# Optimization experiments

Measured on AMD Instinct MI355X. Metric: run time of the kernel, lower is better.

## Reference

```python
import jax, jax.numpy as jnp
import numpy as np

# Fixed feature layout standing in for config.group_tensor_index
IDX_LINE, IDX_LX, IDX_LY, IDX_RX, IDX_RY = 0, 1, 2, 3, 4

B, D, ROUND_DIVIDE = 4_000_000, 16, 8


def setup_inputs() -> dict:
    key = jax.random.key(0)
    k1, k2 = jax.random.split(key)
    z_1 = jax.random.normal(k1, (B, D), dtype=jnp.float32)
    dir = jax.random.uniform(k2, (B, ROUND_DIVIDE), dtype=jnp.float32)
    return {"z_1": z_1, "dir": dir}


def reference(z_1, dir):
    round_divide = dir.shape[1]                 # static
    area_angle = int(180 / round_divide)        # e.g. 22 for 8 zones (matches torch int())
    area_angle_half = area_angle * 0.5

    # direction vector c_2 - c_1 with y flipped (screen coords)
    dx = z_1[:, IDX_RX] - z_1[:, IDX_LX]
    dy = -(z_1[:, IDX_RY] - z_1[:, IDX_LY])

    # cart2pol angle in degrees, mapped to [0, 360)
    phi = jnp.degrees(jnp.arctan2(dy, dx))
    phi = jnp.where(phi < 0, 360.0 + phi, phi)  # == 360 - |phi| for phi<0

    # clockwise shift; .long() truncation == floor since phi >= 0
    phi_clock_shift = (90 + phi.astype(jnp.int32)) % 360

    zone = ((phi_clock_shift.astype(z_1.dtype) + area_angle_half) // area_angle) % round_divide
    zone_id = zone.astype(jnp.int32)            # [B]

    # (dir * one_hot(zone_id)).sum(1) == gather dir at zone_id
    picked = jnp.take_along_axis(dir, zone_id[:, None], axis=1)[:, 0]

    # rows with no line get zero probability
    has_line = z_1[:, IDX_LINE] != 0
    return jnp.where(has_line, picked, jnp.zeros((), dtype=dir.dtype))
```

## Files before the change

### kernel.cpp

```cpp
#include <hip/hip_runtime.h>
#include <math.h>


__device__ __forceinline__ bool is_zone_boundary(int u) {
    return (u <= 251 && (u % 22) == 9) ||
           (u >= 281 && u <= 347 && (u % 22) == 17);
}

__global__ __launch_bounds__(256) void slope_zone_kernel(
    const float* __restrict__ z1,
    const float* __restrict__ dir,
    float* __restrict__ out,
    int n)
{
#pragma clang fp contract(off)
    int i = blockIdx.x * blockDim.x + threadIdx.x;
    if (i >= n) return;

    const float4* zrow = reinterpret_cast<const float4*>(z1 + (size_t)i * 16);
    float4 a = zrow[0];
    float ry = z1[(size_t)i * 16 + 4];

    float dx = a.w - a.y;
    float dy = -(ry - a.z);

    float phi = atan2f(dy, dx) * 57.29577951308232f;
    if (phi < 0.0f) phi = 360.0f + phi;
    int t = (int)phi;

    float fl = (float)t;
    bool near = ((phi - fl)        < 0.01f && is_zone_boundary(t)) ||
                ((fl + 1.0f - phi) < 0.01f && is_zone_boundary(t + 1));
    if (near) {
        float phid = (float)atan2((double)dy, (double)dx) * 57.29577951308232f;
        if (phid < 0.0f) phid = 360.0f + phid;
        t = (int)phid;
    }

    int pcs = (90 + t) % 360;
    int z = (int)(((float)pcs + 11.0f) / 22.0f);
    int zone = z & 7;

    float picked = dir[(size_t)i * 8 + zone];
    out[i] = (a.x != 0.0f) ? picked : 0.0f;
}

extern "C" void kernel_launch(void* const* d_in, const int* in_sizes, int n_in,
                              void* d_out, int out_size, void* d_ws, size_t ws_size,
                              hipStream_t stream) {
    const float* z1  = (const float*)d_in[0];
    const float* dir = (const float*)d_in[1];
    float* out = (float*)d_out;
    int n = out_size;
    int threads = 256;
    int blocks = (n + threads - 1) / threads;
    hipLaunchKernelGGL(slope_zone_kernel, dim3(blocks), dim3(threads), 0, stream,
                       z1, dir, out, n);
}
```

Before: 413.8 us.

## Process four rows per thread with batched vector loads and select-based gather

Each thread now handles four rows strided by n/4, issuing all z1 and full dir-row vector loads before computing, to raise memory-level parallelism. The dependent dir gather is replaced by loading the whole 8-float row and selecting via a bit-indexed select tree. Output uses nontemporal stores. Assumes n divisible by 4 and fetches the full dir row instead of one element.

Result: slower. 422.5 us (+2.1%).

```diff
diff --git a/kernel.cpp b/kernel.cpp
--- a/kernel.cpp
+++ b/kernel.cpp
@@ -1,29 +1,16 @@
 #include <hip/hip_runtime.h>
 #include <math.h>
 
+
+typedef float f32x4 __attribute__((ext_vector_type(4)));
 
 __device__ __forceinline__ bool is_zone_boundary(int u) {
     return (u <= 251 && (u % 22) == 9) ||
            (u >= 281 && u <= 347 && (u % 22) == 17);
 }
 
-__global__ __launch_bounds__(256) void slope_zone_kernel(
-    const float* __restrict__ z1,
-    const float* __restrict__ dir,
-    float* __restrict__ out,
-    int n)
-{
+__device__ __forceinline__ int zone_from(float dx, float dy) {
 #pragma clang fp contract(off)
-    int i = blockIdx.x * blockDim.x + threadIdx.x;
-    if (i >= n) return;
-
-    const float4* zrow = reinterpret_cast<const float4*>(z1 + (size_t)i * 16);
-    float4 a = zrow[0];
-    float ry = z1[(size_t)i * 16 + 4];
-
-    float dx = a.w - a.y;
-    float dy = -(ry - a.z);
-
     float phi = atan2f(dy, dx) * 57.29577951308232f;
     if (phi < 0.0f) phi = 360.0f + phi;
     int t = (int)phi;
@@ -39,10 +26,48 @@
 
     int pcs = (90 + t) % 360;
     int z = (int)(((float)pcs + 11.0f) / 22.0f);
-    int zone = z & 7;
+    return z & 7;
+}
 
-    float picked = dir[(size_t)i * 8 + zone];
-    out[i] = (a.x != 0.0f) ? picked : 0.0f;
+__global__ __launch_bounds__(256) void slope_zone_kernel(
+    const float* __restrict__ z1,
+    const float* __restrict__ dir,
+    float* __restrict__ out,
+    int q)
+{
+    int i = blockIdx.x * blockDim.x + threadIdx.x;
+    if (i >= q) return;
+
+    f32x4 a[4]; float ry[4]; f32x4 dlo[4], dhi[4];
+
+#pragma unroll
+    for (int k = 0; k < 4; ++k) {
+        size_t r = (size_t)i + (size_t)k * (size_t)q;
+        const f32x4* zrow = reinterpret_cast<const f32x4*>(z1 + r * 16);
+        a[k]  = zrow[0];
+        ry[k] = z1[r * 16 + 4];
+        const f32x4* drow = reinterpret_cast<const f32x4*>(dir + r * 8);
+        dlo[k] = drow[0];
+        dhi[k] = drow[1];
+    }
+
+#pragma unroll
+    for (int k = 0; k < 4; ++k) {
+        float dx = a[k][3] - a[k][1];
+        float dy = -(ry[k] - a[k][2]);
+        int zone = zone_from(dx, dy);
+
+        float s0 = (zone & 1) ? dlo[k][1] : dlo[k][0];
+        float s1 = (zone & 1) ? dlo[k][3] : dlo[k][2];
+        float s2 = (zone & 1) ? dhi[k][1] : dhi[k][0];
+        float s3 = (zone & 1) ? dhi[k][3] : dhi[k][2];
+        float t0 = (zone & 2) ? s1 : s0;
+        float t1 = (zone & 2) ? s3 : s2;
+        float picked = (zone & 4) ? t1 : t0;
+
+        float result = (a[k][0] != 0.0f) ? picked : 0.0f;
+        __builtin_nontemporal_store(result, out + (size_t)i + (size_t)k * (size_t)q);
+    }
 }
 
 extern "C" void kernel_launch(void* const* d_in, const int* in_sizes, int n_in,
@@ -52,8 +77,9 @@
     const float* dir = (const float*)d_in[1];
     float* out = (float*)d_out;
     int n = out_size;
+    int q = n / 4;
     int threads = 256;
-    int blocks = (n + threads - 1) / threads;
+    int blocks = (q + threads - 1) / threads;
     hipLaunchKernelGGL(slope_zone_kernel, dim3(blocks), dim3(threads), 0, stream,
-                       z1, dir, out, n);
+                       z1, dir, out, q);
 }
```
